# Kernel optimization log

Hardware: AMD Instinct MI355X
Metric: run time of the kernel (lower is better)

## Reference

```python
import jax, jax.numpy as jnp
import numpy as np
from jax import lax

K = 3  # kernel size
KK = K * K

def setup_inputs() -> dict:
    key = jax.random.key(0)
    ks = jax.random.split(key, 7)
    B, C, H, W = 8, 128, 64, 64
    ck = C * KK  # 1152
    s = 0.05
    return {
        "x":   jax.random.normal(ks[0], (B, C, H, W), jnp.float32),
        "wf":  jax.random.normal(ks[1], (ck, 1, K, K), jnp.float32) * s,
        "bf":  jax.random.normal(ks[2], (ck,), jnp.float32) * s,
        "wc1": jax.random.normal(ks[3], (ck // K, KK), jnp.float32) * s,   # groups=C: [C,3,9]
        "wc2": jax.random.normal(ks[4], (ck, K), jnp.float32) * s,         # groups=C: [C,9,3]
        "wk1": jax.random.normal(ks[5], (ck // 16, C), jnp.float32) * s,   # groups=9: [9,C//16,C]
        "wk2": jax.random.normal(ks[6], (ck, C // 16), jnp.float32) * s,   # groups=9: [9,C,C//16]
    }

def reference(x, wf, bf, wc1, wc2, wk1, wk2):
    B, C, H, W = x.shape
    ck = C * KK
    # kernel_fold: depthwise-expand conv, groups=C, each channel -> 9 channels (c,k order)
    xf = lax.conv_general_dilated(
        x, wf, window_strides=(1, 1), padding=[(1, 1), (1, 1)],
        feature_group_count=C, dimension_numbers=("NCHW", "OIHW", "NCHW"))
    xf = xf + bf[None, :, None, None]              # [B, 9C, H, W]
    # global average pool
    y = jnp.mean(xf, axis=(2, 3))                  # [B, 9C] in (c,k) order
    yck = y.reshape(B, C, KK)                      # [B, C, 9]
    # fc_c branch: grouped 1x1 convs over the 9 kernel taps per channel, then shuffle to (k,c)
    hc = jax.nn.relu(jnp.einsum("bcn,con->bco", yck, wc1.reshape(C, K, KK)))
    ac = jax.nn.sigmoid(jnp.einsum("bco,cno->bcn", hc, wc2.reshape(C, KK, K)))
    ac = ac.transpose(0, 2, 1)                     # ChannelShuffle -> [B, 9, C]
    # fc_k branch: shuffle first to (k,c), grouped 1x1 convs over C channels per kernel tap
    yk = yck.transpose(0, 2, 1)                    # [B, 9, C]
    hk = jax.nn.relu(jnp.einsum("bgc,goc->bgo", yk, wk1.reshape(KK, C // 16, C)))
    ak = jax.nn.sigmoid(jnp.einsum("bgo,gco->bgc", hk, wk2.reshape(KK, C, C // 16)))
    # dual SE gate (flat channel order (k,c), multiplied against xf in (c,k) order, as in torch)
    gate = (ac * ak).reshape(B, ck)                # [B, 9C]
    attn = jnp.broadcast_to(gate[:, :, None, None], xf.shape)
    return xf * gate[:, :, None, None], attn
```

## Files before the change

### kernel.cpp

```cpp
#include <hip/hip_runtime.h>
#include <hip/hip_bf16.h>

typedef float f32x4 __attribute__((ext_vector_type(4)));

static constexpr int Bn  = 8;
static constexpr int Cn  = 128;
static constexpr int KKn = 9;
static constexpr int CKn = Cn * KKn;
static constexpr int PIX = 64 * 64;
static constexpr long long OUT_HALF = (long long)Bn * CKn * PIX;

__global__ __launch_bounds__(256) void k_stats(const float* __restrict__ x,
                                               const float* __restrict__ wf,
                                               const float* __restrict__ bf,
                                               float* __restrict__ yck) {
    const int bc = blockIdx.x;
    const float* xp = x + (size_t)bc * PIX;
    const int t = threadIdx.x;

    float tot = 0.f, r0 = 0.f, r63 = 0.f, c0 = 0.f, c63 = 0.f;
#pragma unroll
    for (int i = 0; i < 4; ++i) {
        int p = (i * 256 + t) * 4;
        float4 v = *reinterpret_cast<const float4*>(xp + p);
        int h = p >> 6;
        int w = p & 63;
        float s = v.x + v.y + v.z + v.w;
        tot += s;
        if (h == 0)  r0  += s;
        if (h == 63) r63 += s;
        if (w == 0)  c0  += v.x;
        if (w == 60) c63 += v.w;
    }

    const int lane = t & 63, wid = t >> 6;
#pragma unroll
    for (int off = 32; off; off >>= 1) {
        tot += __shfl_down(tot, off, 64);
        r0  += __shfl_down(r0,  off, 64);
        r63 += __shfl_down(r63, off, 64);
        c0  += __shfl_down(c0,  off, 64);
        c63 += __shfl_down(c63, off, 64);
    }
    __shared__ float part[4][5];
    __shared__ float S[9];
    if (lane == 0) {
        part[wid][0] = tot; part[wid][1] = r0; part[wid][2] = r63;
        part[wid][3] = c0;  part[wid][4] = c63;
    }
    __syncthreads();
    if (t == 0) {
        float T  = part[0][0] + part[1][0] + part[2][0] + part[3][0];
        float R0 = part[0][1] + part[1][1] + part[2][1] + part[3][1];
        float RB = part[0][2] + part[1][2] + part[2][2] + part[3][2];
        float CL = part[0][3] + part[1][3] + part[2][3] + part[3][3];
        float CR = part[0][4] + part[1][4] + part[2][4] + part[3][4];
        float x00 = xp[0], x0R = xp[63], xB0 = xp[63 * 64], xBR = xp[4095];
#pragma unroll
        for (int dh = -1; dh <= 1; ++dh) {
#pragma unroll
            for (int dw = -1; dw <= 1; ++dw) {
                float rex = (dh == -1) ? RB : (dh == 1 ? R0 : 0.f);
                float cex = (dw == -1) ? CR : (dw == 1 ? CL : 0.f);
                float crn = 0.f;
                if (dh != 0 && dw != 0) {
                    crn = (dh == -1) ? ((dw == -1) ? xBR : xB0)
                                     : ((dw == -1) ? x0R : x00);
                }
                S[(dh + 1) * 3 + (dw + 1)] = T - rex - cex + crn;
            }
        }
    }
    __syncthreads();
    if (t < 9) {
        int o = (bc & 127) * 9 + t;
        const float* wp = wf + o * 9;
        float s = 0.f;
#pragma unroll
        for (int j = 0; j < 9; ++j) s = fmaf(wp[j], S[j], s);
        yck[(size_t)bc * 9 + t] = bf[o] + s * (1.f / 4096.f);
    }
}

__global__ __launch_bounds__(128) void k_gate(const float* __restrict__ yck,
                                              const float* __restrict__ wc1,
                                              const float* __restrict__ wc2,
                                              const float* __restrict__ wk1,
                                              const float* __restrict__ wk2,
                                              float* __restrict__ gate) {
    const int b = blockIdx.x;
    const int c = threadIdx.x;

    __shared__ float ylds[Cn][KKn];
    __shared__ float aclds[Cn][KKn];
    __shared__ float hks[KKn][8];

    const float* yp = yck + ((size_t)b * Cn + c) * KKn;
    float yv[KKn];
#pragma unroll
    for (int k = 0; k < 9; ++k) { yv[k] = yp[k]; ylds[c][k] = yv[k]; }

    float hc[3];
#pragma unroll
    for (int o = 0; o < 3; ++o) {
        float s = 0.f;
#pragma unroll
        for (int n = 0; n < 9; ++n) s = fmaf(yv[n], wc1[(c * 3 + o) * 9 + n], s);
        hc[o] = fmaxf(s, 0.f);
    }
#pragma unroll
    for (int n = 0; n < 9; ++n) {
        float s = 0.f;
#pragma unroll
        for (int o = 0; o < 3; ++o) s = fmaf(hc[o], wc2[(c * 9 + n) * 3 + o], s);
        aclds[c][n] = 1.f / (1.f + expf(-s));
    }
    __syncthreads();

    if (c < 72) {
        int g = c / 8, o = c % 8;
        float s = 0.f;
        for (int cc = 0; cc < Cn; ++cc) s = fmaf(ylds[cc][g], wk1[(g * 8 + o) * Cn + cc], s);
        hks[g][o] = fmaxf(s, 0.f);
    }
    __syncthreads();

#pragma unroll
    for (int g = 0; g < 9; ++g) {
        float s = 0.f;
#pragma unroll
        for (int o = 0; o < 8; ++o) s = fmaf(hks[g][o], wk2[(g * Cn + c) * 8 + o], s);
        float ak = 1.f / (1.f + expf(-s));
        gate[(size_t)b * CKn + g * Cn + c] = aclds[c][g] * ak;
    }
}

__global__ __launch_bounds__(256) void k_out0(const float* __restrict__ x,
                                              const float* __restrict__ wf,
                                              const float* __restrict__ bf,
                                              const float* __restrict__ gate,
                                              float* __restrict__ out0) {
    const int bc = blockIdx.x;
    const int b = bc >> 7;
    const int c = bc & 127;
    const float* xp = x + (size_t)bc * PIX;
    const int t = threadIdx.x;

    __shared__ float wsh[KKn][KKn];
    __shared__ float bsh[KKn];
    __shared__ float gsh[KKn];
    if (t < 81) wsh[t / 9][t % 9] = wf[(size_t)(c * 9) * 9 + t];
    if (t < 9) {
        bsh[t] = bf[c * 9 + t];
        gsh[t] = gate[(size_t)b * CKn + c * 9 + t];
    }
    __syncthreads();

#pragma unroll
    for (int it = 0; it < 4; ++it) {
        int p = it * 1024 + t * 4;
        int h = p >> 6;
        int w = p & 63;

        float rowv[3][6];
#pragma unroll
        for (int dh = 0; dh < 3; ++dh) {
            int hh = h + dh - 1;
            if (hh < 0 || hh > 63) {
#pragma unroll
                for (int j = 0; j < 6; ++j) rowv[dh][j] = 0.f;
            } else {
                const float* rp = xp + hh * 64 + w;
                float4 cen = *reinterpret_cast<const float4*>(rp);
                rowv[dh][1] = cen.x; rowv[dh][2] = cen.y;
                rowv[dh][3] = cen.z; rowv[dh][4] = cen.w;
                rowv[dh][0] = (w > 0)  ? rp[-1] : 0.f;
                rowv[dh][5] = (w < 60) ? rp[4]  : 0.f;
            }
        }

        size_t outBase = (size_t)bc * 9 * PIX + p;
#pragma unroll
        for (int k = 0; k < 9; ++k) {
            float acc0 = bsh[k], acc1 = bsh[k], acc2 = bsh[k], acc3 = bsh[k];
#pragma unroll
            for (int dh = 0; dh < 3; ++dh) {
#pragma unroll
                for (int dw = 0; dw < 3; ++dw) {
                    float wv = wsh[k][dh * 3 + dw];
                    acc0 = fmaf(rowv[dh][0 + dw], wv, acc0);
                    acc1 = fmaf(rowv[dh][1 + dw], wv, acc1);
                    acc2 = fmaf(rowv[dh][2 + dw], wv, acc2);
                    acc3 = fmaf(rowv[dh][3 + dw], wv, acc3);
                }
            }
            float g = gsh[k];
            f32x4 o0 = { acc0 * g, acc1 * g, acc2 * g, acc3 * g };
            *reinterpret_cast<f32x4*>(out0 + outBase + (size_t)k * PIX) = o0;
        }
    }
}

__global__ __launch_bounds__(256) void k_attn(const float* __restrict__ gate,
                                              float* __restrict__ out1) {
    const int blk = blockIdx.x;
    const int t = threadIdx.x;
    const int p0 = blk * 4;

#pragma unroll
    for (int i = 0; i < 4; ++i) {
        const int plane = p0 + i;
        const int b = plane / CKn;
        const int ck = plane - b * CKn;
        const float g = gate[(size_t)b * CKn + ck];
        f32x4 gv = { g, g, g, g };
        float* o = out1 + (size_t)plane * PIX;
#pragma unroll
        for (int j = 0; j < 4; ++j)
            *reinterpret_cast<f32x4*>(o + j * 1024 + t * 4) = gv;
    }
}

extern "C" void kernel_launch(void* const* d_in, const int* in_sizes, int n_in,
                              void* d_out, int out_size, void* d_ws, size_t ws_size,
                              hipStream_t stream) {
    const float* x   = (const float*)d_in[0];
    const float* wf  = (const float*)d_in[1];
    const float* bf  = (const float*)d_in[2];
    const float* wc1 = (const float*)d_in[3];
    const float* wc2 = (const float*)d_in[4];
    const float* wk1 = (const float*)d_in[5];
    const float* wk2 = (const float*)d_in[6];

    float* out0 = (float*)d_out;
    float* out1 = out0 + OUT_HALF;

    float* yck  = (float*)d_ws;
    float* gate = yck + (size_t)Bn * Cn * KKn;

    k_stats<<<Bn * Cn, 256, 0, stream>>>(x, wf, bf, yck);
    k_gate<<<Bn, 128, 0, stream>>>(yck, wc1, wc2, wk1, wk2, gate);
    k_out0<<<Bn * Cn, 256, 0, stream>>>(x, wf, bf, gate, out0);
    k_attn<<<(Bn * CKn) / 4, 256, 0, stream>>>(gate, out1);
}
```

Before: 68.14 us.

## Merge conv-output and attn-fill kernels into one launch, restructure loads

Fuses the depthwise conv output kernel and the attention broadcast fill kernel into a single launch, with extra blocks handling 16 gate planes each. Inside the conv blocks, all input rows for the four pixel groups are loaded up front, then the loops run over output channels, so each channel's nine weights are read once and its output plane is written contiguously. This removes one kernel launch and lets the fill writes overlap with the conv work. In exchange, register pressure rises (72 floats of input held per thread), which may lower occupancy.

```diff
diff --git a/kernel.cpp b/kernel.cpp
--- a/kernel.cpp
+++ b/kernel.cpp
@@ -8,6 +8,8 @@
 static constexpr int KKn = 9;
 static constexpr int CKn = Cn * KKn;
 static constexpr int PIX = 64 * 64;
+static constexpr int NCONV = Bn * Cn;
+static constexpr int NFILL = 576;
 static constexpr long long OUT_HALF = (long long)Bn * CKn * PIX;
 
 __global__ __launch_bounds__(256) void k_stats(const float* __restrict__ x,
@@ -135,16 +137,35 @@
     }
 }
 
-__global__ __launch_bounds__(256) void k_out0(const float* __restrict__ x,
-                                              const float* __restrict__ wf,
-                                              const float* __restrict__ bf,
-                                              const float* __restrict__ gate,
-                                              float* __restrict__ out0) {
+__global__ __launch_bounds__(256) void k_big(const float* __restrict__ x,
+                                             const float* __restrict__ wf,
+                                             const float* __restrict__ bf,
+                                             const float* __restrict__ gate,
+                                             float* __restrict__ out0,
+                                             float* __restrict__ out1) {
+    const int t = threadIdx.x;
+
+    if (blockIdx.x >= NCONV) {
+        const int p0 = (blockIdx.x - NCONV) * 16;
+#pragma unroll 4
+        for (int i = 0; i < 16; ++i) {
+            const int plane = p0 + i;
+            const int b = plane / CKn;
+            const int ck = plane - b * CKn;
+            const float g = gate[(size_t)b * CKn + ck];
+            f32x4 gv = { g, g, g, g };
+            float* o = out1 + (size_t)plane * PIX;
+#pragma unroll
+            for (int j = 0; j < 4; ++j)
+                *reinterpret_cast<f32x4*>(o + j * 1024 + t * 4) = gv;
+        }
+        return;
+    }
+
     const int bc = blockIdx.x;
     const int b = bc >> 7;
     const int c = bc & 127;
     const float* xp = x + (size_t)bc * PIX;
-    const int t = threadIdx.x;
 
     __shared__ float wsh[KKn][KKn];
     __shared__ float bsh[KKn];
@@ -156,68 +177,54 @@
     }
     __syncthreads();
 
+    float rowv[4][3][6];
 #pragma unroll
     for (int it = 0; it < 4; ++it) {
-        int p = it * 1024 + t * 4;
-        int h = p >> 6;
-        int w = p & 63;
-
-        float rowv[3][6];
+        const int p = it * 1024 + t * 4;
+        const int h = p >> 6;
+        const int w = p & 63;
 #pragma unroll
         for (int dh = 0; dh < 3; ++dh) {
-            int hh = h + dh - 1;
+            const int hh = h + dh - 1;
             if (hh < 0 || hh > 63) {
 #pragma unroll
-                for (int j = 0; j < 6; ++j) rowv[dh][j] = 0.f;
+                for (int j = 0; j < 6; ++j) rowv[it][dh][j] = 0.f;
             } else {
                 const float* rp = xp + hh * 64 + w;
                 float4 cen = *reinterpret_cast<const float4*>(rp);
-                rowv[dh][1] = cen.x; rowv[dh][2] = cen.y;
-                rowv[dh][3] = cen.z; rowv[dh][4] = cen.w;
-                rowv[dh][0] = (w > 0)  ? rp[-1] : 0.f;
-                rowv[dh][5] = (w < 60) ? rp[4]  : 0.f;
+                rowv[it][dh][1] = cen.x; rowv[it][dh][2] = cen.y;
+                rowv[it][dh][3] = cen.z; rowv[it][dh][4] = cen.w;
+                rowv[it][dh][0] = (w > 0)  ? rp[-1] : 0.f;
+                rowv[it][dh][5] = (w < 60) ? rp[4]  : 0.f;
             }
         }
-
-        size_t outBase = (size_t)bc * 9 * PIX + p;
-#pragma unroll
-        for (int k = 0; k < 9; ++k) {
-            float acc0 = bsh[k], acc1 = bsh[k], acc2 = bsh[k], acc3 = bsh[k];
+    }
+
+    for (int k = 0; k < 9; ++k) {
+        float wk[9];
+#pragma unroll
+        for (int j = 0; j < 9; ++j) wk[j] = wsh[k][j];
+        const float bk = bsh[k];
+        const float gk = gsh[k];
+        float* o0 = out0 + ((size_t)bc * 9 + k) * PIX;
+
+#pragma unroll
+        for (int it = 0; it < 4; ++it) {
+            float acc0 = bk, acc1 = bk, acc2 = bk, acc3 = bk;
 #pragma unroll
             for (int dh = 0; dh < 3; ++dh) {
 #pragma unroll
                 for (int dw = 0; dw < 3; ++dw) {
-                    float wv = wsh[k][dh * 3 + dw];
-                    acc0 = fmaf(rowv[dh][0 + dw], wv, acc0);
-                    acc1 = fmaf(rowv[dh][1 + dw], wv, acc1);
-                    acc2 = fmaf(rowv[dh][2 + dw], wv, acc2);
-                    acc3 = fmaf(rowv[dh][3 + dw], wv, acc3);
+                    const float wv = wk[dh * 3 + dw];
+                    acc0 = fmaf(rowv[it][dh][0 + dw], wv, acc0);
+                    acc1 = fmaf(rowv[it][dh][1 + dw], wv, acc1);
+                    acc2 = fmaf(rowv[it][dh][2 + dw], wv, acc2);
+                    acc3 = fmaf(rowv[it][dh][3 + dw], wv, acc3);
                 }
             }
-            float g = gsh[k];
-            f32x4 o0 = { acc0 * g, acc1 * g, acc2 * g, acc3 * g };
-            *reinterpret_cast<f32x4*>(out0 + outBase + (size_t)k * PIX) = o0;
-        }
-    }
-}
-
-__global__ __launch_bounds__(256) void k_attn(const float* __restrict__ gate,
-                                              float* __restrict__ out1) {
-    const int blk = blockIdx.x;
-    const int t = threadIdx.x;
-    const int p0 = blk * 4;
-
-#pragma unroll
-    for (int i = 0; i < 4; ++i) {
-        const int plane = p0 + i;
-        const int b = plane / CKn;
-        const int ck = plane - b * CKn;
-        const float g = gate[(size_t)b * CKn + ck];
-        f32x4 gv = { g, g, g, g };
-        float* o = out1 + (size_t)plane * PIX;
-#pragma unroll
-        for (int j = 0; j < 4; ++j)
-            *reinterpret_cast<f32x4*>(o + j * 1024 + t * 4) = gv;
+            f32x4 o = { acc0 * gk, acc1 * gk, acc2 * gk, acc3 * gk };
+            *reinterpret_cast<f32x4*>(o0 + it * 1024 + t * 4) = o;
+        }
     }
 }
 
@@ -240,6 +247,5 @@
 
     k_stats<<<Bn * Cn, 256, 0, stream>>>(x, wf, bf, yck);
     k_gate<<<Bn, 128, 0, stream>>>(yck, wc1, wc2, wk1, wk2, gate);
-    k_out0<<<Bn * Cn, 256, 0, stream>>>(x, wf, bf, gate, out0);
-    k_attn<<<(Bn * CKn) / 4, 256, 0, stream>>>(gate, out1);
-}
+    k_big<<<NCONV + NFILL, 256, 0, stream>>>(x, wf, bf, gate, out0, out1);
+}
```

Result: slower. 73.75 us (+8.2%).

## Fuse SE gate computation into output and attention kernels, drop gate kernel

Applied to the files above, without the earlier changes.

Removes the separate 8-block gate kernel and recomputes the needed gate values redundantly inside each k_out0 and k_attn block from the pooled statistics. This cuts one kernel launch and the serial low-occupancy gate stage between stats and output. In exchange, every block reloads the 1152 pooled values for its batch and does a small MLP (wk1 dot over 128 channels) before writing, which adds latency at the start of each block and repeats weight reads.

```diff
diff --git a/kernel.cpp b/kernel.cpp
--- a/kernel.cpp
+++ b/kernel.cpp
@@ -82,63 +82,15 @@
     }
 }
 
-__global__ __launch_bounds__(128) void k_gate(const float* __restrict__ yck,
+
+__global__ __launch_bounds__(256) void k_out0(const float* __restrict__ x,
+                                              const float* __restrict__ wf,
+                                              const float* __restrict__ bf,
                                               const float* __restrict__ wc1,
                                               const float* __restrict__ wc2,
                                               const float* __restrict__ wk1,
                                               const float* __restrict__ wk2,
-                                              float* __restrict__ gate) {
-    const int b = blockIdx.x;
-    const int c = threadIdx.x;
-
-    __shared__ float ylds[Cn][KKn];
-    __shared__ float aclds[Cn][KKn];
-    __shared__ float hks[KKn][8];
-
-    const float* yp = yck + ((size_t)b * Cn + c) * KKn;
-    float yv[KKn];
-#pragma unroll
-    for (int k = 0; k < 9; ++k) { yv[k] = yp[k]; ylds[c][k] = yv[k]; }
-
-    float hc[3];
-#pragma unroll
-    for (int o = 0; o < 3; ++o) {
-        float s = 0.f;
-#pragma unroll
-        for (int n = 0; n < 9; ++n) s = fmaf(yv[n], wc1[(c * 3 + o) * 9 + n], s);
-        hc[o] = fmaxf(s, 0.f);
-    }
-#pragma unroll
-    for (int n = 0; n < 9; ++n) {
-        float s = 0.f;
-#pragma unroll
-        for (int o = 0; o < 3; ++o) s = fmaf(hc[o], wc2[(c * 9 + n) * 3 + o], s);
-        aclds[c][n] = 1.f / (1.f + expf(-s));
-    }
-    __syncthreads();
-
-    if (c < 72) {
-        int g = c / 8, o = c % 8;
-        float s = 0.f;
-        for (int cc = 0; cc < Cn; ++cc) s = fmaf(ylds[cc][g], wk1[(g * 8 + o) * Cn + cc], s);
-        hks[g][o] = fmaxf(s, 0.f);
-    }
-    __syncthreads();
-
-#pragma unroll
-    for (int g = 0; g < 9; ++g) {
-        float s = 0.f;
-#pragma unroll
-        for (int o = 0; o < 8; ++o) s = fmaf(hks[g][o], wk2[(g * Cn + c) * 8 + o], s);
-        float ak = 1.f / (1.f + expf(-s));
-        gate[(size_t)b * CKn + g * Cn + c] = aclds[c][g] * ak;
-    }
-}
-
-__global__ __launch_bounds__(256) void k_out0(const float* __restrict__ x,
-                                              const float* __restrict__ wf,
-                                              const float* __restrict__ bf,
-                                              const float* __restrict__ gate,
+                                              const float* __restrict__ yck,
                                               float* __restrict__ out0) {
     const int bc = blockIdx.x;
     const int b = bc >> 7;
@@ -146,13 +98,47 @@
     const float* xp = x + (size_t)bc * PIX;
     const int t = threadIdx.x;
 
+    __shared__ float yall[CKn];
+    __shared__ float hks[KKn][8];
     __shared__ float wsh[KKn][KKn];
     __shared__ float bsh[KKn];
     __shared__ float gsh[KKn];
+
+    const float* yb = yck + (size_t)b * CKn;
+    for (int i = t; i < CKn; i += 256) yall[i] = yb[i];
     if (t < 81) wsh[t / 9][t % 9] = wf[(size_t)(c * 9) * 9 + t];
+    if (t < 9)  bsh[t] = bf[c * 9 + t];
+    __syncthreads();
+
+    if (t < 72) {
+        const int k = t >> 3, o = t & 7;
+        const int g = (c * 9 + k) >> 7;
+        const float* wp = wk1 + (g * 8 + o) * Cn;
+        float s = 0.f;
+        for (int cc = 0; cc < Cn; ++cc) s = fmaf(yall[cc * 9 + g], wp[cc], s);
+        hks[k][o] = fmaxf(s, 0.f);
+    }
+    __syncthreads();
+
     if (t < 9) {
-        bsh[t] = bf[c * 9 + t];
-        gsh[t] = gate[(size_t)b * CKn + c * 9 + t];
+        const int flat = c * 9 + t;
+        const int g = flat >> 7, cc = flat & 127;
+        float hc[3];
+#pragma unroll
+        for (int o = 0; o < 3; ++o) {
+            float s = 0.f;
+#pragma unroll
+            for (int n = 0; n < 9; ++n)
+                s = fmaf(yall[cc * 9 + n], wc1[(cc * 3 + o) * 9 + n], s);
+            hc[o] = fmaxf(s, 0.f);
+        }
+        float acv = 0.f;
+#pragma unroll
+        for (int o = 0; o < 3; ++o) acv = fmaf(hc[o], wc2[(cc * 9 + g) * 3 + o], acv);
+        float akv = 0.f;
+#pragma unroll
+        for (int o = 0; o < 8; ++o) akv = fmaf(hks[t][o], wk2[(g * Cn + cc) * 8 + o], akv);
+        gsh[t] = (1.f / (1.f + expf(-acv))) * (1.f / (1.f + expf(-akv)));
     }
     __syncthreads();
 
@@ -201,20 +187,66 @@
     }
 }
 
-__global__ __launch_bounds__(256) void k_attn(const float* __restrict__ gate,
+__global__ __launch_bounds__(256) void k_attn(const float* __restrict__ wc1,
+                                              const float* __restrict__ wc2,
+                                              const float* __restrict__ wk1,
+                                              const float* __restrict__ wk2,
+                                              const float* __restrict__ yck,
                                               float* __restrict__ out1) {
     const int blk = blockIdx.x;
     const int t = threadIdx.x;
     const int p0 = blk * 4;
+    const int b  = p0 / CKn;
+    const int f0 = p0 - b * CKn;
+    const int g  = f0 >> 7;
+    const int c0 = f0 & 127;
+
+    __shared__ float yall[CKn];
+    __shared__ float hko[8];
+    __shared__ float acs[4];
+    __shared__ float gs[4];
+
+    const float* yb = yck + (size_t)b * CKn;
+    for (int i = t; i < CKn; i += 256) yall[i] = yb[i];
+    __syncthreads();
+
+    if (t < 8) {
+        const float* wp = wk1 + (g * 8 + t) * Cn;
+        float s = 0.f;
+        for (int cc = 0; cc < Cn; ++cc) s = fmaf(yall[cc * 9 + g], wp[cc], s);
+        hko[t] = fmaxf(s, 0.f);
+    } else if (t >= 64 && t < 68) {
+        const int cc = c0 + (t - 64);
+        float hc[3];
+#pragma unroll
+        for (int o = 0; o < 3; ++o) {
+            float s = 0.f;
+#pragma unroll
+            for (int n = 0; n < 9; ++n)
+                s = fmaf(yall[cc * 9 + n], wc1[(cc * 3 + o) * 9 + n], s);
+            hc[o] = fmaxf(s, 0.f);
+        }
+        float acv = 0.f;
+#pragma unroll
+        for (int o = 0; o < 3; ++o) acv = fmaf(hc[o], wc2[(cc * 9 + g) * 3 + o], acv);
+        acs[t - 64] = 1.f / (1.f + expf(-acv));
+    }
+    __syncthreads();
+
+    if (t < 4) {
+        const int cc = c0 + t;
+        float akv = 0.f;
+#pragma unroll
+        for (int o = 0; o < 8; ++o) akv = fmaf(hko[o], wk2[(g * Cn + cc) * 8 + o], akv);
+        gs[t] = acs[t] * (1.f / (1.f + expf(-akv)));
+    }
+    __syncthreads();
 
 #pragma unroll
     for (int i = 0; i < 4; ++i) {
-        const int plane = p0 + i;
-        const int b = plane / CKn;
-        const int ck = plane - b * CKn;
-        const float g = gate[(size_t)b * CKn + ck];
-        f32x4 gv = { g, g, g, g };
-        float* o = out1 + (size_t)plane * PIX;
+        const float gv1 = gs[i];
+        f32x4 gv = { gv1, gv1, gv1, gv1 };
+        float* o = out1 + (size_t)(p0 + i) * PIX;
 #pragma unroll
         for (int j = 0; j < 4; ++j)
             *reinterpret_cast<f32x4*>(o + j * 1024 + t * 4) = gv;
@@ -235,11 +267,9 @@
     float* out0 = (float*)d_out;
     float* out1 = out0 + OUT_HALF;
 
-    float* yck  = (float*)d_ws;
-    float* gate = yck + (size_t)Bn * Cn * KKn;
+    float* yck = (float*)d_ws;
 
     k_stats<<<Bn * Cn, 256, 0, stream>>>(x, wf, bf, yck);
-    k_gate<<<Bn, 128, 0, stream>>>(yck, wc1, wc2, wk1, wk2, gate);
-    k_out0<<<Bn * Cn, 256, 0, stream>>>(x, wf, bf, gate, out0);
-    k_attn<<<(Bn * CKn) / 4, 256, 0, stream>>>(gate, out1);
-}
+    k_out0<<<Bn * Cn, 256, 0, stream>>>(x, wf, bf, wc1, wc2, wk1, wk2, yck, out0);
+    k_attn<<<(Bn * CKn) / 4, 256, 0, stream>>>(wc1, wc2, wk1, wk2, yck, out1);
+}
```

After: 73.35 us. 7.6% more time.
